# Kernel optimization log

Measured on AMD Instinct MI355X. Metric: run time of the kernel, lower is better.

## Reference

```python
import jax, jax.numpy as jnp
import numpy as np

NUM_HEADS = 8
DIM_HEAD = 64
SCALE = DIM_HEAD * NUM_HEADS  # q *= dim_head * num_heads, as in the source


def setup_inputs() -> dict:
    key = jax.random.key(0)
    k1, k2, k3, k4 = jax.random.split(key, 4)
    B, C, H, W = 8, 64, 32, 32
    x = jax.random.normal(k1, (B, C, H, W), dtype=jnp.float32)
    # 1x1 conv == matmul over channels; small init keeps post-scale logits sane
    w_qkv = jax.random.normal(k2, (3 * NUM_HEADS * DIM_HEAD, C), dtype=jnp.float32) * 0.02
    rel_h = jax.random.normal(k3, (2 * H - 1, DIM_HEAD), dtype=jnp.float32) * 0.02
    rel_w = jax.random.normal(k4, (2 * W - 1, DIM_HEAD), dtype=jnp.float32) * 0.02
    return {"x": x, "w_qkv": w_qkv, "rel_h": rel_h, "rel_w": rel_w}


def _rel_indices(H, W):
    # flattened 2D grid positions
    pos_y = np.repeat(np.arange(H), W)  # [HW]
    pos_x = np.tile(np.arange(W), H)    # [HW]
    rel_y = pos_y[None, :] - pos_y[:, None] + (H - 1)  # [HW, HW] in [0, 2H-2]
    rel_x = pos_x[None, :] - pos_x[:, None] + (W - 1)  # [HW, HW] in [0, 2W-2]
    return jnp.asarray(rel_y), jnp.asarray(rel_x)


def reference(x, w_qkv, rel_h, rel_w):
    B, C, H, W = x.shape
    n = H * W
    # 1x1 conv (bias=False) -> per-pixel matmul
    xf = x.reshape(B, C, n)                              # b c n
    qkv = jnp.einsum('oc,bcn->bon', w_qkv, xf)           # b (3 h d) n
    q, k, v = jnp.split(qkv, 3, axis=1)
    def to_heads(t):  # b (h d) n -> b h n d
        return t.reshape(B, NUM_HEADS, DIM_HEAD, n).transpose(0, 1, 3, 2)
    q, k, v = to_heads(q), to_heads(k), to_heads(v)
    q = q * SCALE  # scale applied before QK^T AND before pos bias (in-place in torch)

    sim = jnp.einsum('bhid,bhjd->bhij', q, k)            # [B, h, n, n]

    # relative position bias: q_i . rel_h[dy] + q_i . rel_w[dx]
    logits_h = jnp.einsum('bhid,rd->bhir', q, rel_h)     # [B, h, n, 2H-1]
    logits_w = jnp.einsum('bhid,rd->bhir', q, rel_w)     # [B, h, n, 2W-1]
    rel_y, rel_x = _rel_indices(H, W)                    # [n, n] each
    i_idx = jnp.arange(n)[:, None]                       # [n, 1]
    bias = logits_h[:, :, i_idx, rel_y] + logits_w[:, :, i_idx, rel_x]  # [B,h,n,n]

    attn = jax.nn.softmax(sim + bias, axis=-1)
    out = jnp.einsum('bhij,bhjd->bhid', attn, v)         # [B, h, n, d]
    out = out.transpose(0, 1, 3, 2).reshape(B, NUM_HEADS * DIM_HEAD, H, W)
    return out
```

## Files before the change

### kernel.cpp

```cpp
#include <hip/hip_runtime.h>
#include <hip/hip_bf16.h>
#include <hip/hip_fp16.h>

typedef _Float16 h8 __attribute__((ext_vector_type(8)));
typedef _Float16 h2 __attribute__((ext_vector_type(2)));
typedef unsigned short us8 __attribute__((ext_vector_type(8)));
typedef float f4 __attribute__((ext_vector_type(4)));

#define NH 8
#define DH 64
#define NPIX 1024
#define CIN 64
#define NBH 64
#define QSCALE (512.0f * 1.44269504f)
#define LOSCALE 2048.0f
#define INV_LOSCALE (1.0f / 2048.0f)
#define DTHR 12.0f

__device__ __forceinline__ void gload_lds16(const void* g, void* lds) {
  __builtin_amdgcn_global_load_lds(
      (const __attribute__((address_space(1))) void*)g,
      (__attribute__((address_space(3))) void*)lds, 16, 0, 0);
}

__device__ __forceinline__ float fexp2(float x) {
#if __has_builtin(__builtin_amdgcn_exp2f)
  return __builtin_amdgcn_exp2f(x);
#else
  return exp2f(x);
#endif
}

__device__ __forceinline__ unsigned pk16(float a, float b) {
  auto r = __builtin_amdgcn_cvt_pkrtz(a, b);
  union { decltype(r) h; unsigned u; } x;
  x.h = r;
  return x.u;
}

__device__ __forceinline__ f4 max4(f4 a, f4 b) {
  f4 r;
  r[0] = fmaxf(a[0], b[0]); r[1] = fmaxf(a[1], b[1]);
  r[2] = fmaxf(a[2], b[2]); r[3] = fmaxf(a[3], b[3]);
  return r;
}

__global__ __launch_bounds__(256) void qkv_mfma(
    const float* __restrict__ x, const float* __restrict__ wqkv,
    _Float16* __restrict__ Qh, _Float16* __restrict__ Ql,
    _Float16* __restrict__ Kh, _Float16* __restrict__ Kl,
    _Float16* __restrict__ Vv) {
  __shared__ __align__(16) char QS[49152];
  char* Wh = QS;
  char* Wl = QS + 16384;
  char* Xh = QS + 32768;
  char* Xl = QS + 40960;

  const int tid = threadIdx.x;
  const int lane = tid & 63;
  const int w = tid >> 6;
  const int c = lane & 15;
  const int g = lane >> 4;
  const int o0 = blockIdx.x * 128;
  const int p0 = blockIdx.y * 64;
  const int b = blockIdx.z;

  #pragma unroll
  for (int it = 0; it < 4; ++it) {
    int task = tid + it * 256;
    int oct = task & 7, o = task >> 3;
    const f4* wr = (const f4*)(wqkv + (size_t)(o0 + o) * CIN + oct * 8);
    f4 wa = wr[0], wb = wr[1];
    h8 hi, lo;
    #pragma unroll
    for (int e = 0; e < 8; ++e) {
      float v = e < 4 ? wa[e] : wb[e - 4];
      _Float16 h = (_Float16)v;
      hi[e] = h;
      lo[e] = (_Float16)((v - (float)h) * LOSCALE);
    }
    int byo = o * 128 + ((oct ^ (o & 7)) << 4);
    *(h8*)(Wh + byo) = hi;
    *(h8*)(Wl + byo) = lo;
  }
  {
    int kp = tid & 31;
    int pgrp = tid >> 5;
    const float* xr0 = x + ((size_t)b * CIN + 2 * kp) * NPIX + p0 + pgrp * 8;
    const float* xr1 = xr0 + NPIX;
    f4 a0 = *(const f4*)xr0, a1 = *(const f4*)(xr0 + 4);
    f4 b0 = *(const f4*)xr1, b1 = *(const f4*)(xr1 + 4);
    int oct = kp >> 2;
    int slot4 = (kp & 3) * 4;
    #pragma unroll
    for (int e = 0; e < 8; ++e) {
      float v0 = e < 4 ? a0[e] : a1[e - 4];
      float v1 = e < 4 ? b0[e] : b1[e - 4];
      _Float16 h0 = (_Float16)v0, h1 = (_Float16)v1;
      float l0f = (v0 - (float)h0) * LOSCALE;
      float l1f = (v1 - (float)h1) * LOSCALE;
      int p = pgrp * 8 + e;
      int byo = p * 128 + ((oct ^ (p & 7)) << 4) + slot4;
      union { h2 h; unsigned u; } uh, ul;
      uh.h[0] = h0; uh.h[1] = h1;
      ul.h[0] = (_Float16)l0f; ul.h[1] = (_Float16)l1f;
      *(unsigned*)(Xh + byo) = uh.u;
      *(unsigned*)(Xl + byo) = ul.u;
    }
  }
  __syncthreads();

  f4 zf = {0.f, 0.f, 0.f, 0.f};
  f4 acc[2][4], cor[2][4];
  #pragma unroll
  for (int oi = 0; oi < 2; ++oi)
    #pragma unroll
    for (int pi = 0; pi < 4; ++pi) { acc[oi][pi] = zf; cor[oi][pi] = zf; }

  const int ob = w * 32;
  #pragma unroll
  for (int kh = 0; kh < 2; ++kh) {
    h8 ah[2], al[2], bh[4], bl[4];
    #pragma unroll
    for (int oi = 0; oi < 2; ++oi) {
      int orow = ob + ((c >> 2) << 3) + (c & 3) + oi * 4;
      int ch = (((kh * 4 + g) ^ (orow & 7)) << 4);
      ah[oi] = *(const h8*)(Wh + orow * 128 + ch);
      al[oi] = *(const h8*)(Wl + orow * 128 + ch);
    }
    #pragma unroll
    for (int pi = 0; pi < 4; ++pi) {
      int prow = pi * 16 + c;
      int ch = (((kh * 4 + g) ^ (prow & 7)) << 4);
      bh[pi] = *(const h8*)(Xh + prow * 128 + ch);
      bl[pi] = *(const h8*)(Xl + prow * 128 + ch);
    }
    __builtin_amdgcn_s_setprio(1);
    #pragma unroll
    for (int oi = 0; oi < 2; ++oi)
      #pragma unroll
      for (int pi = 0; pi < 4; ++pi) {
        acc[oi][pi] = __builtin_amdgcn_mfma_f32_16x16x32_f16(ah[oi], bh[pi], acc[oi][pi], 0, 0, 0);
        cor[oi][pi] = __builtin_amdgcn_mfma_f32_16x16x32_f16(ah[oi], bl[pi], cor[oi][pi], 0, 0, 0);
        cor[oi][pi] = __builtin_amdgcn_mfma_f32_16x16x32_f16(al[oi], bh[pi], cor[oi][pi], 0, 0, 0);
      }
    __builtin_amdgcn_s_setprio(0);
  }

  const int part = o0 >> 9;
  const float scl = part == 0 ? QSCALE : 1.0f;
  _Float16* dsth = part == 0 ? Qh : (part == 1 ? Kh : Vv);
  _Float16* dstl = part == 0 ? Ql : (part == 1 ? Kl : nullptr);
  #pragma unroll
  for (int pi = 0; pi < 4; ++pi) {
    int obase = o0 + ob + 8 * g;
    int h = (obase >> 6) & 7;
    int d = obase & 63;
    int p_abs = p0 + pi * 16 + c;
    size_t off = (((size_t)(b * NH + h)) * NPIX + p_abs) * DH + d;
    h8 hv, lv;
    #pragma unroll
    for (int oi = 0; oi < 2; ++oi)
      #pragma unroll
      for (int reg = 0; reg < 4; ++reg) {
        float v = (acc[oi][pi][reg] + cor[oi][pi][reg] * INV_LOSCALE) * scl;
        _Float16 hh = (_Float16)v;
        hv[oi * 4 + reg] = hh;
        lv[oi * 4 + reg] = (_Float16)(v - (float)hh);
      }
    *(h8*)(dsth + off) = hv;
    if (dstl) *(h8*)(dstl + off) = lv;
  }
}

__global__ __launch_bounds__(256, 2) void attn_mfma(
    const _Float16* __restrict__ Qh, const _Float16* __restrict__ Ql,
    const _Float16* __restrict__ Kh, const _Float16* __restrict__ Kl,
    const _Float16* __restrict__ V,
    const float* __restrict__ rel_h, const float* __restrict__ rel_w,
    float* __restrict__ out) {
  __shared__ __align__(16) char SMem[65536];
  char* SP = SMem + 49152;
  _Float16* LHc = (_Float16*)(SMem + 57344);
  _Float16* LWT = (_Float16*)(SMem + 32768);
  float* OT = (float*)SMem;

  const int tid = threadIdx.x;
  const int lane = tid & 63;
  const int w = tid >> 6;
  const int wu = __builtin_amdgcn_readfirstlane(w);
  const int c = lane & 15;
  const int g = lane >> 4;
  const int bx = blockIdx.x;
  const int bh = ((bx & 7) << 3) | ((bx >> 3) & 7);
  const int i0 = (bx >> 6) << 7;
  const int swz = (c & 7) << 4;

  const _Float16* Qhg = Qh + (size_t)bh * NPIX * DH;
  const _Float16* Qlg = Ql + (size_t)bh * NPIX * DH;
  const _Float16* Khg = Kh + (size_t)bh * NPIX * DH;
  const _Float16* Klg = Kl + (size_t)bh * NPIX * DH;
  const _Float16* Vg  = V  + (size_t)bh * NPIX * DH;

  const h8* Qr0h = (const h8*)(Qhg + (size_t)(i0 + w * 32 + c) * DH);
  const h8* Qr0l = (const h8*)(Qlg + (size_t)(i0 + w * 32 + c) * DH);
  const h8* Qr1h = (const h8*)(Qhg + (size_t)(i0 + w * 32 + 16 + c) * DH);
  const h8* Qr1l = (const h8*)(Qlg + (size_t)(i0 + w * 32 + 16 + c) * DH);
  h8 q0h[2] = {Qr0h[g], Qr0h[4 + g]};
  h8 q0l[2] = {Qr0l[g], Qr0l[4 + g]};
  h8 q1h[2] = {Qr1h[g], Qr1h[4 + g]};
  h8 q1l[2] = {Qr1l[g], Qr1l[4 + g]};

  const int s0i = wu * 128 + lane;
  const int s1i = s0i + 64;
  const int ko0 = (s0i >> 3) * 128 + (((s0i & 7) ^ ((s0i >> 3) & 7)) << 4);
  const int ko1 = (s1i >> 3) * 128 + (((s1i & 7) ^ ((s1i >> 3) & 7)) << 4);

  #pragma unroll
  for (int it = 0; it < 2; ++it) {
    int task = tid + it * 256;
    int oct = task & 7, s = task >> 3;
    int ss = s < 63 ? s : 62;
    const float* sh = rel_h + (size_t)ss * DH + oct * 8;
    const float* sw = rel_w + (size_t)ss * DH + oct * 8;
    h8 hh, ww;
    #pragma unroll
    for (int e = 0; e < 8; ++e) {
      hh[e] = (_Float16)sh[e];
      ww[e] = (_Float16)sw[e];
    }
    int byo = s * 128 + ((oct ^ (s & 7)) << 4);
    *(h8*)(SMem + byo) = hh;
    *(h8*)(SMem + 16384 + byo) = ww;
  }
  __syncthreads();

  const int yi = (i0 + w * 32) >> 5;
  f4 zf = {0.f, 0.f, 0.f, 0.f};
  #pragma unroll
  for (int rs = 0; rs < 2; ++rs) {
    f4 lhD[4], lwD[4];
    #pragma unroll
    for (int st = 0; st < 4; ++st) { lhD[st] = zf; lwD[st] = zf; }
    #pragma unroll
    for (int kh = 0; kh < 2; ++kh) {
      h8 bq = rs ? q1h[kh] : q0h[kh];
      h8 bl = rs ? q1l[kh] : q0l[kh];
      #pragma unroll
      for (int st = 0; st < 4; ++st) {
        int srow = st * 16 + c;
        int chb = srow * 128 + (((kh * 4 + g) ^ (srow & 7)) << 4);
        h8 ra = *(const h8*)(SMem + chb);
        h8 wa = *(const h8*)(SMem + 16384 + chb);
        lhD[st] = __builtin_amdgcn_mfma_f32_16x16x32_f16(ra, bq, lhD[st], 0, 0, 0);
        lhD[st] = __builtin_amdgcn_mfma_f32_16x16x32_f16(ra, bl, lhD[st], 0, 0, 0);
        lwD[st] = __builtin_amdgcn_mfma_f32_16x16x32_f16(wa, bq, lwD[st], 0, 0, 0);
        lwD[st] = __builtin_amdgcn_mfma_f32_16x16x32_f16(wa, bl, lwD[st], 0, 0, 0);
      }
    }
    int lrow = w * 32 + rs * 16 + c;
    #pragma unroll
    for (int st = 0; st < 4; ++st)
      #pragma unroll
      for (int reg = 0; reg < 4; ++reg) {
        int s = st * 16 + 4 * g + reg;
        int k = s - 31 + yi;
        if (k >= 0 && k < 32)
          LHc[(k >> 1) * 256 + lrow * 2 + (k & 1)] = (_Float16)lhD[st][reg];
        LWT[lrow * 64 + s] = (_Float16)lwD[st][reg];
      }
  }
  __syncthreads();

  float lwp0[8], lwp1[8];
  #pragma unroll
  for (int jbp = 0; jbp < 2; ++jbp)
    #pragma unroll
    for (int reg = 0; reg < 4; ++reg) {
      lwp0[jbp * 4 + reg] = (float)LWT[(w * 32 + c) * 64 + 31 + jbp * 16 + 4 * g + reg - c];
      lwp1[jbp * 4 + reg] = (float)LWT[(w * 32 + 16 + c) * 64 + 31 + jbp * 16 + 4 * g + reg - 16 - c];
    }
  __syncthreads();

  {
    gload_lds16((const char*)Khg + ko0, SMem + wu * 2048);
    gload_lds16((const char*)Khg + ko1, SMem + wu * 2048 + 1024);
    gload_lds16((const char*)Klg + ko0, SMem + 16384 + wu * 2048);
    gload_lds16((const char*)Klg + ko1, SMem + 16384 + wu * 2048 + 1024);
    int jp = tid & 31, dd = tid >> 5;
    const h8* vr = (const h8*)(Vg + (size_t)(2 * jp) * DH);
    h8 v0 = vr[dd], v1 = vr[8 + dd];
    us8 u0 = *(const us8*)&v0, u1 = *(const us8*)&v1;
    #pragma unroll
    for (int e = 0; e < 8; ++e) {
      int d = dd * 8 + e;
      unsigned int val = (unsigned int)u0[e] | ((unsigned int)u1[e] << 16);
      *(unsigned int*)(SMem + 32768 + d * 128 + (((jp >> 2) ^ (d & 7)) << 4) + (jp & 3) * 4) = val;
    }
  }
  __syncthreads();

  float m0 = -1e30f, m1 = -1e30f, lp0 = 0.f, lp1 = 0.f;
  f4 o0_[4], o1_[4];
  #pragma unroll
  for (int dt = 0; dt < 4; ++dt) { o0_[dt] = zf; o1_[dt] = zf; }

  int cur = 0;
  #pragma unroll 1
  for (int t = 0; t < 16; ++t) {
    char* Kc  = SMem + cur * 8192;
    char* KLc = SMem + 16384 + cur * 8192;
    char* Vc  = SMem + 32768 + cur * 8192;
    const int nxt = cur ^ 1;
    const bool pre = t < 15;
    const int jp = tid & 31, dd = tid >> 5;
    h8 v0 = {}, v1 = {};
    if (pre) {
      const char* kg  = (const char*)Khg + (size_t)(t + 1) * 8192;
      const char* klg = (const char*)Klg + (size_t)(t + 1) * 8192;
      gload_lds16(kg + ko0, SMem + nxt * 8192 + wu * 2048);
      gload_lds16(kg + ko1, SMem + nxt * 8192 + wu * 2048 + 1024);
      gload_lds16(klg + ko0, SMem + 16384 + nxt * 8192 + wu * 2048);
      gload_lds16(klg + ko1, SMem + 16384 + nxt * 8192 + wu * 2048 + 1024);
      const h8* vr = (const h8*)(Vg + (size_t)((t + 1) * 64 + 2 * jp) * DH);
      v0 = vr[dd];
      v1 = vr[8 + dd];
    }

    f4 s0[4], s1[4];
    #pragma unroll
    for (int jb = 0; jb < 4; ++jb) { s0[jb] = zf; s1[jb] = zf; }
    #pragma unroll
    for (int kh = 0; kh < 2; ++kh) {
      h8 b0h = q0h[kh], b0l = q0l[kh], b1h = q1h[kh], b1l = q1l[kh];
      #pragma unroll
      for (int jb = 0; jb < 4; ++jb) {
        int chb = (jb * 16 + c) * 128 + (((kh * 4 + g) ^ (c & 7)) << 4);
        h8 ah = *(const h8*)(Kc + chb);
        h8 al = *(const h8*)(KLc + chb);
        __builtin_amdgcn_s_setprio(1);
        s0[jb] = __builtin_amdgcn_mfma_f32_16x16x32_f16(ah, b0h, s0[jb], 0, 0, 0);
        s0[jb] = __builtin_amdgcn_mfma_f32_16x16x32_f16(al, b0h, s0[jb], 0, 0, 0);
        s0[jb] = __builtin_amdgcn_mfma_f32_16x16x32_f16(ah, b0l, s0[jb], 0, 0, 0);
        s1[jb] = __builtin_amdgcn_mfma_f32_16x16x32_f16(ah, b1h, s1[jb], 0, 0, 0);
        s1[jb] = __builtin_amdgcn_mfma_f32_16x16x32_f16(al, b1h, s1[jb], 0, 0, 0);
        s1[jb] = __builtin_amdgcn_mfma_f32_16x16x32_f16(ah, b1l, s1[jb], 0, 0, 0);
        __builtin_amdgcn_s_setprio(0);
      }
    }

    auto finish = [&](f4* s_, const float* lwp, float& m_s, float& lp,
                      f4* o_, int rs) {
      int rr = w * 32 + rs * 16 + c;
      h2 lhu = *(const h2*)(LHc + t * 256 + rr * 2);
      float lh0 = (float)lhu[0], lh1 = (float)lhu[1];
      #pragma unroll
      for (int jb = 0; jb < 4; ++jb) {
        float lhv = (jb >> 1) ? lh1 : lh0;
        #pragma unroll
        for (int reg = 0; reg < 4; ++reg)
          s_[jb][reg] += lwp[(jb & 1) * 4 + reg] + lhv;
      }
      f4 ef = max4(max4(s_[0], s_[1]), max4(s_[2], s_[3]));
      float mx = fmaxf(fmaxf(ef[0], ef[1]), fmaxf(ef[2], ef[3]));
      mx = fmaxf(mx, __shfl_xor(mx, 16, 64));
      mx = fmaxf(mx, __shfl_xor(mx, 32, 64));
      bool sk = mx <= m_s + DTHR;
      if (!__all(sk)) {
        float mn = fmaxf(m_s, mx);
        float corr = fexp2(m_s - mn);
        m_s = mn;
        lp *= corr;
        #pragma unroll
        for (int dt = 0; dt < 4; ++dt)
          #pragma unroll
          for (int reg = 0; reg < 4; ++reg)
            o_[dt][reg] *= corr;
      }
      f4 psum = zf;
      char* pbse = SP + w * 2048 + c * 128;
      #pragma unroll
      for (int jb = 0; jb < 4; ++jb) {
        f4 p;
        #pragma unroll
        for (int reg = 0; reg < 4; ++reg) p[reg] = fexp2(s_[jb][reg] - m_s);
        psum[0] += p[0]; psum[1] += p[1]; psum[2] += p[2]; psum[3] += p[3];
        unsigned long long u = (unsigned long long)pk16(p[0], p[1]) |
                               ((unsigned long long)pk16(p[2], p[3]) << 32);
        *(unsigned long long*)(pbse + ((jb * 32 + 8 * g) ^ swz)) = u;
      }
      lp += (psum[0] + psum[1]) + (psum[2] + psum[3]);
    };

    finish(s0, lwp0, m0, lp0, o0_, 0);
    __builtin_amdgcn_wave_barrier();

    h8 vbr[2][4];
    #pragma unroll
    for (int kh = 0; kh < 2; ++kh) {
      int och = ((kh * 4 + g) ^ (c & 7)) << 4;
      h8 pb = *(const h8*)(SP + w * 2048 + c * 128 + och);
      __builtin_amdgcn_s_setprio(1);
      #pragma unroll
      for (int dt = 0; dt < 4; ++dt) {
        vbr[kh][dt] = *(const h8*)(Vc + (dt * 16 + c) * 128 + och);
        o0_[dt] = __builtin_amdgcn_mfma_f32_16x16x32_f16(vbr[kh][dt], pb, o0_[dt], 0, 0, 0);
      }
      __builtin_amdgcn_s_setprio(0);
    }

    finish(s1, lwp1, m1, lp1, o1_, 1);
    __builtin_amdgcn_wave_barrier();

    #pragma unroll
    for (int kh = 0; kh < 2; ++kh) {
      int och = ((kh * 4 + g) ^ (c & 7)) << 4;
      h8 pb = *(const h8*)(SP + w * 2048 + c * 128 + och);
      __builtin_amdgcn_s_setprio(1);
      #pragma unroll
      for (int dt = 0; dt < 4; ++dt)
        o1_[dt] = __builtin_amdgcn_mfma_f32_16x16x32_f16(vbr[kh][dt], pb, o1_[dt], 0, 0, 0);
      __builtin_amdgcn_s_setprio(0);
    }

    if (pre) {
      us8 u0 = *(const us8*)&v0, u1 = *(const us8*)&v1;
      char* Vn = SMem + 32768 + nxt * 8192;
      #pragma unroll
      for (int e = 0; e < 8; ++e) {
        int d = dd * 8 + e;
        unsigned int val = (unsigned int)u0[e] | ((unsigned int)u1[e] << 16);
        *(unsigned int*)(Vn + d * 128 + (((jp >> 2) ^ (d & 7)) << 4) + (jp & 3) * 4) = val;
      }
    }
    __syncthreads();
    cur = nxt;
  }

  float a0 = lp0;
  a0 += __shfl_xor(a0, 16, 64);
  a0 += __shfl_xor(a0, 32, 64);
  float r0 = __builtin_amdgcn_rcpf(a0);
  float a1 = lp1;
  a1 += __shfl_xor(a1, 16, 64);
  a1 += __shfl_xor(a1, 32, 64);
  float r1 = __builtin_amdgcn_rcpf(a1);
  #pragma unroll
  for (int dt = 0; dt < 4; ++dt)
    #pragma unroll
    for (int reg = 0; reg < 4; ++reg) {
      int d = dt * 16 + 4 * g + reg;
      int sw = (d & 7) << 3;
      int il0 = w * 32 + c;
      OT[d * 128 + (il0 ^ sw)] = o0_[dt][reg] * r0;
      OT[d * 128 + ((il0 + 16) ^ sw)] = o1_[dt][reg] * r1;
    }
  __syncthreads();
  #pragma unroll
  for (int it = 0; it < 8; ++it) {
    int task = tid + it * 256;
    int rq = task & 31, d = task >> 5;
    f4 vv = *(const f4*)&OT[d * 128 + ((rq * 4) ^ ((d & 7) << 3))];
    *(f4*)(out + (((size_t)bh * 64 + d) << 10) + i0 + rq * 4) = vv;
  }
}

extern "C" void kernel_launch(void* const* d_in, const int* in_sizes, int n_in,
                              void* d_out, int out_size, void* d_ws, size_t ws_size,
                              hipStream_t stream) {
  const float* x  = (const float*)d_in[0];
  const float* wq = (const float*)d_in[1];
  const float* rh = (const float*)d_in[2];
  const float* rw = (const float*)d_in[3];
  float* out = (float*)d_out;

  const size_t sz = (size_t)NBH * NPIX * DH;
  _Float16* Qh = (_Float16*)d_ws;
  _Float16* Ql = Qh + sz;
  _Float16* Kh = Ql + sz;
  _Float16* Kl = Kh + sz;
  _Float16* V  = Kl + sz;

  qkv_mfma<<<dim3(12, 16, 8), 256, 0, stream>>>(x, wq, Qh, Ql, Kh, Kl, V);
  attn_mfma<<<dim3(512), 256, 0, stream>>>(Qh, Ql, Kh, Kl, V, rh, rw, out);
}
```

Measured before the change: 78.85 us.

## Switch attention inner loop from 16x16x32 to 32x32x16 MFMA tiles

Rewrites the attention kernel's QK^T and PV stages to use 32x32x16 MFMA instructions, so each wave handles its 32 query rows as one tile instead of two 16-row halves. The softmax bookkeeping (row max, running sum, rescale) becomes a single state per lane, and the per-wave P staging buffer and the LDS layout grow (LDS raised to 72KB). This is meant to cut MFMA issue count, LDS reads per FLOP and duplicated softmax work. The cost is more accumulator registers per wave and more shared memory, which may limit occupancy at two blocks per CU.

```diff
diff --git a/kernel.cpp b/kernel.cpp
--- a/kernel.cpp
+++ b/kernel.cpp
@@ -6,6 +6,7 @@
 typedef _Float16 h2 __attribute__((ext_vector_type(2)));
 typedef unsigned short us8 __attribute__((ext_vector_type(8)));
 typedef float f4 __attribute__((ext_vector_type(4)));
+typedef float f16v __attribute__((ext_vector_type(16)));
 
 #define NH 8
 #define DH 64
@@ -36,13 +37,6 @@
   union { decltype(r) h; unsigned u; } x;
   x.h = r;
   return x.u;
-}
-
-__device__ __forceinline__ f4 max4(f4 a, f4 b) {
-  f4 r;
-  r[0] = fmaxf(a[0], b[0]); r[1] = fmaxf(a[1], b[1]);
-  r[2] = fmaxf(a[2], b[2]); r[3] = fmaxf(a[3], b[3]);
-  return r;
 }
 
 __global__ __launch_bounds__(256) void qkv_mfma(
@@ -179,9 +173,8 @@
     const _Float16* __restrict__ V,
     const float* __restrict__ rel_h, const float* __restrict__ rel_w,
     float* __restrict__ out) {
-  __shared__ __align__(16) char SMem[65536];
-  char* SP = SMem + 49152;
-  _Float16* LHc = (_Float16*)(SMem + 57344);
+  __shared__ __align__(16) char SMem[73728];
+  _Float16* LHc = (_Float16*)(SMem + 65536);
   _Float16* LWT = (_Float16*)(SMem + 32768);
   float* OT = (float*)SMem;
 
@@ -191,10 +184,12 @@
   const int wu = __builtin_amdgcn_readfirstlane(w);
   const int c = lane & 15;
   const int g = lane >> 4;
+  const int il = lane & 31;
+  const int hi = lane >> 5;
   const int bx = blockIdx.x;
   const int bh = ((bx & 7) << 3) | ((bx >> 3) & 7);
   const int i0 = (bx >> 6) << 7;
-  const int swz = (c & 7) << 4;
+  char* SPw = SMem + 49152 + w * 4096;
 
   const _Float16* Qhg = Qh + (size_t)bh * NPIX * DH;
   const _Float16* Qlg = Ql + (size_t)bh * NPIX * DH;
@@ -272,14 +267,23 @@
   }
   __syncthreads();
 
-  float lwp0[8], lwp1[8];
-  #pragma unroll
-  for (int jbp = 0; jbp < 2; ++jbp)
-    #pragma unroll
-    for (int reg = 0; reg < 4; ++reg) {
-      lwp0[jbp * 4 + reg] = (float)LWT[(w * 32 + c) * 64 + 31 + jbp * 16 + 4 * g + reg - c];
-      lwp1[jbp * 4 + reg] = (float)LWT[(w * 32 + 16 + c) * 64 + 31 + jbp * 16 + 4 * g + reg - 16 - c];
-    }
+  float lwp[16];
+  {
+    int r = w * 32 + il;
+    #pragma unroll
+    for (int reg = 0; reg < 16; ++reg) {
+      int jl = (reg & 3) + 8 * (reg >> 2) + 4 * hi;
+      lwp[reg] = (float)LWT[r * 64 + 31 + jl - il];
+    }
+  }
+  const h8* Qmh = (const h8*)(Qhg + (size_t)(i0 + w * 32 + il) * DH);
+  const h8* Qml = (const h8*)(Qlg + (size_t)(i0 + w * 32 + il) * DH);
+  h8 qmh[4], qml[4];
+  #pragma unroll
+  for (int kb = 0; kb < 4; ++kb) {
+    qmh[kb] = Qmh[2 * kb + hi];
+    qml[kb] = Qml[2 * kb + hi];
+  }
   __syncthreads();
 
   {
@@ -300,11 +304,12 @@
   }
   __syncthreads();
 
-  float m0 = -1e30f, m1 = -1e30f, lp0 = 0.f, lp1 = 0.f;
-  f4 o0_[4], o1_[4];
-  #pragma unroll
-  for (int dt = 0; dt < 4; ++dt) { o0_[dt] = zf; o1_[dt] = zf; }
-
+  float m_s = -1e30f, lp = 0.f;
+  f16v O0 = {0.f}, O1 = {0.f};
+  #pragma unroll
+  for (int e = 0; e < 16; ++e) { O0[e] = 0.f; O1[e] = 0.f; }
+
+  const int swl = (il & 7);
   int cur = 0;
   #pragma unroll 1
   for (int t = 0; t < 16; ++t) {
@@ -327,43 +332,43 @@
       v1 = vr[8 + dd];
     }
 
-    f4 s0[4], s1[4];
-    #pragma unroll
-    for (int jb = 0; jb < 4; ++jb) { s0[jb] = zf; s1[jb] = zf; }
-    #pragma unroll
-    for (int kh = 0; kh < 2; ++kh) {
-      h8 b0h = q0h[kh], b0l = q0l[kh], b1h = q1h[kh], b1l = q1l[kh];
-      #pragma unroll
-      for (int jb = 0; jb < 4; ++jb) {
-        int chb = (jb * 16 + c) * 128 + (((kh * 4 + g) ^ (c & 7)) << 4);
-        h8 ah = *(const h8*)(Kc + chb);
-        h8 al = *(const h8*)(KLc + chb);
-        __builtin_amdgcn_s_setprio(1);
-        s0[jb] = __builtin_amdgcn_mfma_f32_16x16x32_f16(ah, b0h, s0[jb], 0, 0, 0);
-        s0[jb] = __builtin_amdgcn_mfma_f32_16x16x32_f16(al, b0h, s0[jb], 0, 0, 0);
-        s0[jb] = __builtin_amdgcn_mfma_f32_16x16x32_f16(ah, b0l, s0[jb], 0, 0, 0);
-        s1[jb] = __builtin_amdgcn_mfma_f32_16x16x32_f16(ah, b1h, s1[jb], 0, 0, 0);
-        s1[jb] = __builtin_amdgcn_mfma_f32_16x16x32_f16(al, b1h, s1[jb], 0, 0, 0);
-        s1[jb] = __builtin_amdgcn_mfma_f32_16x16x32_f16(ah, b1l, s1[jb], 0, 0, 0);
-        __builtin_amdgcn_s_setprio(0);
-      }
-    }
-
-    auto finish = [&](f4* s_, const float* lwp, float& m_s, float& lp,
-                      f4* o_, int rs) {
-      int rr = w * 32 + rs * 16 + c;
-      h2 lhu = *(const h2*)(LHc + t * 256 + rr * 2);
+    f16v S0 = O0 * 0.f, S1 = O0 * 0.f;
+    #pragma unroll
+    for (int e = 0; e < 16; ++e) { S0[e] = 0.f; S1[e] = 0.f; }
+    #pragma unroll
+    for (int kb = 0; kb < 4; ++kb) {
+      int chb0 = il * 128 + (((2 * kb + hi) ^ swl) << 4);
+      int chb1 = chb0 + 32 * 128;
+      h8 a0h = *(const h8*)(Kc + chb0);
+      h8 a0l = *(const h8*)(KLc + chb0);
+      h8 a1h = *(const h8*)(Kc + chb1);
+      h8 a1l = *(const h8*)(KLc + chb1);
+      __builtin_amdgcn_s_setprio(1);
+      S0 = __builtin_amdgcn_mfma_f32_32x32x16_f16(a0h, qmh[kb], S0, 0, 0, 0);
+      S0 = __builtin_amdgcn_mfma_f32_32x32x16_f16(a0l, qmh[kb], S0, 0, 0, 0);
+      S0 = __builtin_amdgcn_mfma_f32_32x32x16_f16(a0h, qml[kb], S0, 0, 0, 0);
+      S1 = __builtin_amdgcn_mfma_f32_32x32x16_f16(a1h, qmh[kb], S1, 0, 0, 0);
+      S1 = __builtin_amdgcn_mfma_f32_32x32x16_f16(a1l, qmh[kb], S1, 0, 0, 0);
+      S1 = __builtin_amdgcn_mfma_f32_32x32x16_f16(a1h, qml[kb], S1, 0, 0, 0);
+      __builtin_amdgcn_s_setprio(0);
+    }
+
+    {
+      int r = w * 32 + il;
+      h2 lhu = *(const h2*)(LHc + t * 256 + r * 2);
       float lh0 = (float)lhu[0], lh1 = (float)lhu[1];
       #pragma unroll
-      for (int jb = 0; jb < 4; ++jb) {
-        float lhv = (jb >> 1) ? lh1 : lh0;
-        #pragma unroll
-        for (int reg = 0; reg < 4; ++reg)
-          s_[jb][reg] += lwp[(jb & 1) * 4 + reg] + lhv;
-      }
-      f4 ef = max4(max4(s_[0], s_[1]), max4(s_[2], s_[3]));
-      float mx = fmaxf(fmaxf(ef[0], ef[1]), fmaxf(ef[2], ef[3]));
-      mx = fmaxf(mx, __shfl_xor(mx, 16, 64));
+      for (int reg = 0; reg < 16; ++reg) {
+        S0[reg] += lwp[reg] + lh0;
+        S1[reg] += lwp[reg] + lh1;
+      }
+      float v8[8];
+      #pragma unroll
+      for (int e = 0; e < 8; ++e)
+        v8[e] = fmaxf(fmaxf(S0[e], S0[e + 8]), fmaxf(S1[e], S1[e + 8]));
+      float w0 = fmaxf(fmaxf(v8[0], v8[1]), fmaxf(v8[2], v8[3]));
+      float w1 = fmaxf(fmaxf(v8[4], v8[5]), fmaxf(v8[6], v8[7]));
+      float mx = fmaxf(w0, w1);
       mx = fmaxf(mx, __shfl_xor(mx, 32, 64));
       bool sk = mx <= m_s + DTHR;
       if (!__all(sk)) {
@@ -372,54 +377,44 @@
         m_s = mn;
         lp *= corr;
         #pragma unroll
-        for (int dt = 0; dt < 4; ++dt)
-          #pragma unroll
-          for (int reg = 0; reg < 4; ++reg)
-            o_[dt][reg] *= corr;
-      }
-      f4 psum = zf;
-      char* pbse = SP + w * 2048 + c * 128;
-      #pragma unroll
-      for (int jb = 0; jb < 4; ++jb) {
-        f4 p;
-        #pragma unroll
-        for (int reg = 0; reg < 4; ++reg) p[reg] = fexp2(s_[jb][reg] - m_s);
-        psum[0] += p[0]; psum[1] += p[1]; psum[2] += p[2]; psum[3] += p[3];
-        unsigned long long u = (unsigned long long)pk16(p[0], p[1]) |
-                               ((unsigned long long)pk16(p[2], p[3]) << 32);
-        *(unsigned long long*)(pbse + ((jb * 32 + 8 * g) ^ swz)) = u;
-      }
-      lp += (psum[0] + psum[1]) + (psum[2] + psum[3]);
-    };
-
-    finish(s0, lwp0, m0, lp0, o0_, 0);
+        for (int e = 0; e < 16; ++e) { O0[e] *= corr; O1[e] *= corr; }
+      }
+      float sum = 0.f;
+      char* pbse = SPw + il * 128 + hi * 8;
+      #pragma unroll
+      for (int a = 0; a < 4; ++a) {
+        float p0 = fexp2(S0[4 * a + 0] - m_s);
+        float p1 = fexp2(S0[4 * a + 1] - m_s);
+        float p2 = fexp2(S0[4 * a + 2] - m_s);
+        float p3 = fexp2(S0[4 * a + 3] - m_s);
+        sum += (p0 + p1) + (p2 + p3);
+        *(unsigned long long*)(pbse + ((a ^ swl) << 4)) =
+            (unsigned long long)pk16(p0, p1) | ((unsigned long long)pk16(p2, p3) << 32);
+      }
+      #pragma unroll
+      for (int a = 0; a < 4; ++a) {
+        float p0 = fexp2(S1[4 * a + 0] - m_s);
+        float p1 = fexp2(S1[4 * a + 1] - m_s);
+        float p2 = fexp2(S1[4 * a + 2] - m_s);
+        float p3 = fexp2(S1[4 * a + 3] - m_s);
+        sum += (p0 + p1) + (p2 + p3);
+        *(unsigned long long*)(pbse + (((4 + a) ^ swl) << 4)) =
+            (unsigned long long)pk16(p0, p1) | ((unsigned long long)pk16(p2, p3) << 32);
+      }
+      lp += sum;
+    }
     __builtin_amdgcn_wave_barrier();
 
-    h8 vbr[2][4];
-    #pragma unroll
-    for (int kh = 0; kh < 2; ++kh) {
-      int och = ((kh * 4 + g) ^ (c & 7)) << 4;
-      h8 pb = *(const h8*)(SP + w * 2048 + c * 128 + och);
+    #pragma unroll
+    for (int jkb = 0; jkb < 4; ++jkb) {
+      int ci = 2 * jkb + hi;
+      int och = ((ci ^ swl) << 4);
+      h8 pb = *(const h8*)(SPw + il * 128 + och);
       __builtin_amdgcn_s_setprio(1);
-      #pragma unroll
-      for (int dt = 0; dt < 4; ++dt) {
-        vbr[kh][dt] = *(const h8*)(Vc + (dt * 16 + c) * 128 + och);
-        o0_[dt] = __builtin_amdgcn_mfma_f32_16x16x32_f16(vbr[kh][dt], pb, o0_[dt], 0, 0, 0);
-      }
-      __builtin_amdgcn_s_setprio(0);
-    }
-
-    finish(s1, lwp1, m1, lp1, o1_, 1);
-    __builtin_amdgcn_wave_barrier();
-
-    #pragma unroll
-    for (int kh = 0; kh < 2; ++kh) {
-      int och = ((kh * 4 + g) ^ (c & 7)) << 4;
-      h8 pb = *(const h8*)(SP + w * 2048 + c * 128 + och);
-      __builtin_amdgcn_s_setprio(1);
-      #pragma unroll
-      for (int dt = 0; dt < 4; ++dt)
-        o1_[dt] = __builtin_amdgcn_mfma_f32_16x16x32_f16(vbr[kh][dt], pb, o1_[dt], 0, 0, 0);
+      h8 av0 = *(const h8*)(Vc + il * 128 + och);
+      h8 av1 = *(const h8*)(Vc + (32 + il) * 128 + och);
+      O0 = __builtin_amdgcn_mfma_f32_32x32x16_f16(av0, pb, O0, 0, 0, 0);
+      O1 = __builtin_amdgcn_mfma_f32_32x32x16_f16(av1, pb, O1, 0, 0, 0);
       __builtin_amdgcn_s_setprio(0);
     }
 
@@ -437,24 +432,19 @@
     cur = nxt;
   }
 
-  float a0 = lp0;
-  a0 += __shfl_xor(a0, 16, 64);
-  a0 += __shfl_xor(a0, 32, 64);
-  float r0 = __builtin_amdgcn_rcpf(a0);
-  float a1 = lp1;
-  a1 += __shfl_xor(a1, 16, 64);
-  a1 += __shfl_xor(a1, 32, 64);
-  float r1 = __builtin_amdgcn_rcpf(a1);
-  #pragma unroll
-  for (int dt = 0; dt < 4; ++dt)
-    #pragma unroll
-    for (int reg = 0; reg < 4; ++reg) {
-      int d = dt * 16 + 4 * g + reg;
-      int sw = (d & 7) << 3;
-      int il0 = w * 32 + c;
-      OT[d * 128 + (il0 ^ sw)] = o0_[dt][reg] * r0;
-      OT[d * 128 + ((il0 + 16) ^ sw)] = o1_[dt][reg] * r1;
-    }
+  float lt = lp + __shfl_xor(lp, 32, 64);
+  float rr = __builtin_amdgcn_rcpf(lt);
+  {
+    int r = w * 32 + il;
+    #pragma unroll
+    for (int reg = 0; reg < 16; ++reg) {
+      int dl = (reg & 3) + 8 * (reg >> 2) + 4 * hi;
+      int d0 = dl;
+      int d1 = 32 + dl;
+      OT[d0 * 128 + (r ^ ((d0 & 7) << 3))] = O0[reg] * rr;
+      OT[d1 * 128 + (r ^ ((d1 & 7) << 3))] = O1[reg] * rr;
+    }
+  }
   __syncthreads();
   #pragma unroll
   for (int it = 0; it < 8; ++it) {
```

Result: faster. 76.01 us (-3.6%).
